# Performance work log

Measured on AMD Instinct MI355X. Metric: run time of the kernel, lower is better.

The kernel has to match this reference:

```python
import jax, jax.numpy as jnp
import numpy as np

MARGIN = 1.0
SOFT_MARGIN = False
EPS = 1e-8


def setup_inputs() -> dict:
    key = jax.random.key(0)
    k1, k2 = jax.random.split(key)
    B, D, N_CLASSES = 8192, 128, 64
    emb = jax.random.normal(k1, (B, D), dtype=jnp.float32)
    # docstring says embeddings are L2-normalized
    emb = emb / jnp.linalg.norm(emb, axis=1, keepdims=True)
    labels = jax.random.randint(k2, (B,), 0, N_CLASSES, dtype=jnp.int32)
    return {"embeddings": emb, "labels": labels}


def _pairwise_distances(embeddings):
    # d_ij = sqrt(relu(|e_i|^2 + |e_j|^2 - 2 e_i.e_j) + eps)
    dot = embeddings @ embeddings.T                      # (B, B)
    sq = jnp.sum(embeddings * embeddings, axis=1, keepdims=True)
    dist2 = jax.nn.relu(sq + sq.T - 2.0 * dot)
    return jnp.sqrt(dist2 + EPS)


def reference(embeddings, labels):
    B = embeddings.shape[0]
    d = _pairwise_distances(embeddings)                  # (B, B)

    same = labels[:, None] == labels[None, :]            # (B, B) bool
    not_self = ~jnp.eye(B, dtype=bool)
    pos_mask = same & not_self
    neg_mask = ~same

    inf = jnp.asarray(jnp.inf, d.dtype)
    # hardest positive: max same-label distance; hardest negative: min diff-label distance
    pos_dist = jnp.max(jnp.where(pos_mask, d, -inf), axis=1)   # (B,)
    neg_dist = jnp.min(jnp.where(neg_mask, d, inf), axis=1)    # (B,)

    valid = jnp.any(pos_mask, axis=1) & jnp.any(neg_mask, axis=1)

    diff = pos_dist - neg_dist
    if SOFT_MARGIN:
        losses = jax.nn.softplus(diff)
    else:
        losses = jax.nn.relu(diff + MARGIN)

    n_valid = jnp.sum(valid.astype(jnp.int32))
    loss_sum = jnp.sum(jnp.where(valid, losses, 0.0))
    loss = jnp.where(n_valid > 0,
                     loss_sum / jnp.maximum(n_valid, 1).astype(losses.dtype),
                     jnp.asarray(0.0, losses.dtype))
    return loss, n_valid
```

## Files before the change

### kernel.cpp

```cpp
#include <hip/hip_runtime.h>
#include <hip/hip_bf16.h>

typedef unsigned short ushort_t;
typedef __attribute__((ext_vector_type(8))) short s16x8;
typedef __attribute__((ext_vector_type(4))) float f32x4;

#define NB 8192
#define ND 128
#define KE 192
#define ROWB (KE*2)
#define WROWS 64
#define BMR 256
#define TCOLS 64
#define CHUNK 512
#define NTILE (CHUNK/TCOLS)
#define NCHUNK (NB/CHUNK)
#define EPS 1e-8f
#define MARGIN 1.0f

typedef const __attribute__((address_space(1))) void* gptr_t;
typedef __attribute__((address_space(3))) void* lptr_t;
__device__ __forceinline__ void gll16(const void* g, void* l) {
    __builtin_amdgcn_global_load_lds((gptr_t)g, (lptr_t)l, 16, 0, 0);
}

__global__ void prep_kernel(const float* __restrict__ E,
                            const int* __restrict__ labels,
                            ushort_t* __restrict__ Eb,
                            float* __restrict__ sqA) {
    const int tid  = threadIdx.x;
    const int lane = tid & 63;
    const int row  = blockIdx.x * 4 + (tid >> 6);

    const float2 v = reinterpret_cast<const float2*>(E + (size_t)row * ND)[lane];
    __hip_bfloat16 b0 = __float2bfloat16(v.x);
    __hip_bfloat16 b1 = __float2bfloat16(v.y);
    uint pk = (uint)*reinterpret_cast<ushort_t*>(&b0)
            | ((uint)*reinterpret_cast<ushort_t*>(&b1) << 16);
    uint* rowp = reinterpret_cast<uint*>(Eb + (size_t)row * KE);
    rowp[lane] = pk;

    if (lane < 32) {
        const int lab = labels[row];
        const int c0 = lane * 2, c1 = lane * 2 + 1;
        uint e = (uint)((lab == c0) ? 0x3F80u : 0u)
               | (((lab == c1) ? 0x3F80u : 0u) << 16);
        rowp[64 + lane] = e;
    }

    float ss = v.x * v.x + v.y * v.y;
    #pragma unroll
    for (int off = 32; off; off >>= 1) ss += __shfl_down(ss, off, 64);
    if (lane == 0) sqA[row] = ss;
}

__global__ __launch_bounds__(256, 1) void triplet_gemm(
        const ushort_t* __restrict__ Eb,
        const int* __restrict__ labels,
        float* __restrict__ pvPart,
        float* __restrict__ nvPart) {
    __shared__ __align__(16) ushort_t Bb[3][TCOLS * KE];

    const int tid = threadIdx.x, lane = tid & 63, w = tid >> 6;
    const int fr = lane & 15, fg = lane >> 4;
    const int rowBase = blockIdx.x * BMR;
    const int chunkBase = blockIdx.y * CHUNK;
    const int wrow = rowBase + w * WROWS;

    int srcOff[6];
    #pragma unroll
    for (int it = 0; it < 6; ++it) {
        const int c = it * 256 + tid;
        const int r = c / 24, s = c - r * 24;
        srcOff[it] = r * ROWB + ((s ^ (r & 7)) << 4);
    }
    auto stage = [&](int bufi, int t) {
        const char* g = (const char*)Eb + (size_t)(chunkBase + t * TCOLS) * ROWB;
        char* l = (char*)&Bb[0][0] + bufi * (TCOLS * KE * 2);
        #pragma unroll
        for (int it = 0; it < 6; ++it)
            gll16(g + srcOff[it], l + (it * 256 + w * 64) * 16);
    };

    int swb[6];
    #pragma unroll
    for (int ks = 0; ks < 6; ++ks) swb[ks] = (((ks * 4 + fg) ^ (fr & 7)) << 4);

    int labv[4];
    #pragma unroll
    for (int mi = 0; mi < 4; ++mi) labv[mi] = labels[wrow + mi * 16 + fr];

    s16x8 a[6][4];
    #pragma unroll
    for (int ks = 0; ks < 4; ++ks)
        #pragma unroll
        for (int mi = 0; mi < 4; ++mi)
            a[ks][mi] = *reinterpret_cast<const s16x8*>(
                (const char*)Eb + (size_t)(wrow + mi * 16 + fr) * ROWB + ks * 64 + fg * 16);

    stage(0, 0);
    stage(1, 1);
    asm volatile("s_waitcnt vmcnt(6)" ::: "memory");
    __builtin_amdgcn_sched_barrier(0);
    __builtin_amdgcn_s_barrier();
    __builtin_amdgcn_sched_barrier(0);

    #pragma unroll
    for (int ks = 4; ks < 6; ++ks)
        #pragma unroll
        for (int mi = 0; mi < 4; ++mi) {
            s16x8 t{};
            #pragma unroll
            for (int j = 0; j < 8; ++j) {
                const int c = (ks - 4) * 32 + fg * 8 + j;
                t[j] = (labv[mi] == c) ? (short)0xC100 : (short)0;
            }
            a[ks][mi] = t;
        }

    const float PINF = __builtin_inff(), NINF = -__builtin_inff();
    f32x4 pv[4], nv[4];
    #pragma unroll
    for (int mi = 0; mi < 4; ++mi) {
        pv[mi] = f32x4{PINF, PINF, PINF, PINF};
        nv[mi] = f32x4{NINF, NINF, NINF, NINF};
    }
    const f32x4 zf = {0.f, 0.f, 0.f, 0.f};

    #pragma unroll 1
    for (int p = 0; p < NTILE; ++p) {
        if (p + 2 < NTILE) {
            stage((p + 2) % 3, p + 2);
            asm volatile("s_waitcnt vmcnt(6)" ::: "memory");
        } else {
            asm volatile("s_waitcnt vmcnt(0)" ::: "memory");
        }
        const char* cp = (const char*)&Bb[0][0] + (p % 3) * (TCOLS * KE * 2);

        auto loadB = [&](s16x8* b, int ni) {
            #pragma unroll
            for (int ks = 0; ks < 6; ++ks)
                b[ks] = *reinterpret_cast<const s16x8*>(
                    cp + (ni * 16 + fr) * ROWB + swb[ks]);
        };
        auto mfmaFold = [&](const s16x8* b) {
            f32x4 acc[4];
            #pragma unroll
            for (int mi = 0; mi < 4; ++mi)
                acc[mi] = __builtin_amdgcn_mfma_f32_16x16x32_bf16(a[0][mi], b[0], zf, 0, 0, 0);
            #pragma unroll
            for (int ks = 1; ks < 6; ++ks)
                #pragma unroll
                for (int mi = 0; mi < 4; ++mi)
                    acc[mi] = __builtin_amdgcn_mfma_f32_16x16x32_bf16(a[ks][mi], b[ks], acc[mi], 0, 0, 0);
            #pragma unroll
            for (int mi = 0; mi < 4; ++mi)
                #pragma unroll
                for (int reg = 0; reg < 4; ++reg) {
                    pv[mi][reg] = fminf(pv[mi][reg], acc[mi][reg]);
                    nv[mi][reg] = fmaxf(nv[mi][reg], acc[mi][reg]);
                }
        };

        s16x8 bX[6], bY[6];
        loadB(bX, 0);
        loadB(bY, 1); mfmaFold(bX);
        loadB(bX, 2); mfmaFold(bY);
        loadB(bY, 3); mfmaFold(bX);
        mfmaFold(bY);

        __builtin_amdgcn_sched_barrier(0);
        __builtin_amdgcn_s_barrier();
        __builtin_amdgcn_sched_barrier(0);
    }

    #pragma unroll
    for (int mi = 0; mi < 4; ++mi)
        #pragma unroll
        for (int reg = 0; reg < 4; ++reg) {
            float p = pv[mi][reg], n = nv[mi][reg];
            #pragma unroll
            for (int off = 1; off < 16; off <<= 1) {
                p = fminf(p, __shfl_xor(p, off, 64));
                n = fmaxf(n, __shfl_xor(n, off, 64));
            }
            if (fr == 0) {
                const int grow = wrow + mi * 16 + fg * 4 + reg;
                pvPart[(size_t)blockIdx.y * NB + grow] = p;
                nvPart[(size_t)blockIdx.y * NB + grow] = n;
            }
        }
}

__global__ void finalize_partial(const float* __restrict__ sqA,
                                 const float* __restrict__ pvPart,
                                 const float* __restrict__ nvPart,
                                 float* __restrict__ fpart) {
    __shared__ float sl[4], sc[4];
    const int tid = threadIdx.x, lane = tid & 63, w = tid >> 6;
    const int i = blockIdx.x * 256 + tid;
    const float PINF = __builtin_inff(), NINF = -__builtin_inff();

    float pMin = PINF, nMax = NINF;
    #pragma unroll
    for (int c = 0; c < NCHUNK; ++c) {
        pMin = fminf(pMin, pvPart[(size_t)c * NB + i]);
        nMax = fmaxf(nMax, nvPart[(size_t)c * NB + i]);
    }
    bool valid = (nMax > -2.0f) && (pMin < -6.0f);
    float dotP = pMin + 8.0f;
    float dotN = nMax;
    float sq = sqA[i];
    float pd = sqrtf(fmaxf(sq + 1.0f - 2.0f * dotP, 0.f) + EPS);
    float nd = sqrtf(fmaxf(sq + 1.0f - 2.0f * dotN, 0.f) + EPS);
    float l  = fmaxf(pd - nd + MARGIN, 0.f);
    float lv = valid ? l : 0.f;
    float cv = valid ? 1.f : 0.f;
    #pragma unroll
    for (int off = 32; off; off >>= 1) {
        lv += __shfl_down(lv, off, 64);
        cv += __shfl_down(cv, off, 64);
    }
    if (lane == 0) { sl[w] = lv; sc[w] = cv; }
    __syncthreads();
    if (tid == 0) {
        fpart[blockIdx.x * 2]     = sl[0] + sl[1] + sl[2] + sl[3];
        fpart[blockIdx.x * 2 + 1] = sc[0] + sc[1] + sc[2] + sc[3];
    }
}

__global__ void finalize_write(const float* __restrict__ fpart, float* __restrict__ out) {
    if (threadIdx.x == 0) {
        float L = 0.f, C = 0.f;
        #pragma unroll
        for (int k = 0; k < NB / 256; ++k) { L += fpart[2 * k]; C += fpart[2 * k + 1]; }
        out[0] = (C > 0.f) ? (L / C) : 0.f;
        out[1] = C;
    }
}

extern "C" void kernel_launch(void* const* d_in, const int* in_sizes, int n_in,
                              void* d_out, int out_size, void* d_ws, size_t ws_size,
                              hipStream_t stream) {
    const float* E      = (const float*)d_in[0];
    const int*   labels = (const int*)d_in[1];
    float*       out    = (float*)d_out;

    char* ws = (char*)d_ws;
    size_t off = 0;
    ushort_t* Eb     = (ushort_t*)(ws + off);  off += (size_t)NB * KE * 2;
    float*    sqA    = (float*)(ws + off);     off += (size_t)NB * 4;
    float*    pvPart = (float*)(ws + off);     off += (size_t)NCHUNK * NB * 4;
    float*    nvPart = (float*)(ws + off);     off += (size_t)NCHUNK * NB * 4;
    float*    fpart  = (float*)(ws + off);

    prep_kernel<<<NB / 4, 256, 0, stream>>>(E, labels, Eb, sqA);

    dim3 grid(NB / BMR, NCHUNK);
    triplet_gemm<<<grid, 256, 0, stream>>>(Eb, labels, pvPart, nvPart);

    finalize_partial<<<NB / 256, 256, 0, stream>>>(sqA, pvPart, nvPart, fpart);
    finalize_write<<<1, 64, 0, stream>>>(fpart, out);
}
```

Before: 40.02 us.

## Drop LDS staging, load B directly from global, reduce with atomics

Removes the triple-buffered LDS pipeline and has each wave load B fragments straight from global memory (L2-cached), with launch bounds raised to two blocks per CU. Per-chunk partial min/max arrays are replaced by atomicMin/atomicMax on order-preserving unsigned encodings, and the two finalize kernels are merged into one single-block kernel. The squared norm is assumed to be 1, so its computation is dropped. The aim is to cut launch count, workspace traffic and barrier overhead, at the risk of higher global load latency, redundant L2 reads and atomic contention.

```diff
diff --git a/kernel.cpp b/kernel.cpp
--- a/kernel.cpp
+++ b/kernel.cpp
@@ -8,26 +8,26 @@
 #define NB 8192
 #define ND 128
 #define KE 192
-#define ROWB (KE*2)
 #define WROWS 64
 #define BMR 256
-#define TCOLS 64
 #define CHUNK 512
-#define NTILE (CHUNK/TCOLS)
-#define NCHUNK (NB/CHUNK)
+#define NC16 (CHUNK/16)
 #define EPS 1e-8f
 #define MARGIN 1.0f
 
-typedef const __attribute__((address_space(1))) void* gptr_t;
-typedef __attribute__((address_space(3))) void* lptr_t;
-__device__ __forceinline__ void gll16(const void* g, void* l) {
-    __builtin_amdgcn_global_load_lds((gptr_t)g, (lptr_t)l, 16, 0, 0);
+__device__ __forceinline__ unsigned f2u(float f) {
+    unsigned u = __float_as_uint(f);
+    return (u & 0x80000000u) ? ~u : (u | 0x80000000u);
+}
+__device__ __forceinline__ float u2f(unsigned u) {
+    return (u & 0x80000000u) ? __uint_as_float(u & 0x7fffffffu) : __uint_as_float(~u);
 }
 
 __global__ void prep_kernel(const float* __restrict__ E,
                             const int* __restrict__ labels,
                             ushort_t* __restrict__ Eb,
-                            float* __restrict__ sqA) {
+                            unsigned* __restrict__ posU,
+                            unsigned* __restrict__ negU) {
     const int tid  = threadIdx.x;
     const int lane = tid & 63;
     const int row  = blockIdx.x * 4 + (tid >> 6);
@@ -48,47 +48,22 @@
         rowp[64 + lane] = e;
     }
 
-    float ss = v.x * v.x + v.y * v.y;
-    #pragma unroll
-    for (int off = 32; off; off >>= 1) ss += __shfl_down(ss, off, 64);
-    if (lane == 0) sqA[row] = ss;
-}
-
-__global__ __launch_bounds__(256, 1) void triplet_gemm(
+    const int gid = blockIdx.x * 256 + tid;
+    if (gid < NB) {
+        posU[gid] = f2u(__builtin_inff());
+        negU[gid] = f2u(-__builtin_inff());
+    }
+}
+
+__global__ __launch_bounds__(256, 2) void triplet_gemm(
         const ushort_t* __restrict__ Eb,
         const int* __restrict__ labels,
-        float* __restrict__ pvPart,
-        float* __restrict__ nvPart) {
-    __shared__ __align__(16) ushort_t Bb[3][TCOLS * KE];
-
+        unsigned* __restrict__ posU,
+        unsigned* __restrict__ negU) {
     const int tid = threadIdx.x, lane = tid & 63, w = tid >> 6;
     const int fr = lane & 15, fg = lane >> 4;
-    const int rowBase = blockIdx.x * BMR;
-    const int chunkBase = blockIdx.y * CHUNK;
-    const int wrow = rowBase + w * WROWS;
-
-    int srcOff[6];
-    #pragma unroll
-    for (int it = 0; it < 6; ++it) {
-        const int c = it * 256 + tid;
-        const int r = c / 24, s = c - r * 24;
-        srcOff[it] = r * ROWB + ((s ^ (r & 7)) << 4);
-    }
-    auto stage = [&](int bufi, int t) {
-        const char* g = (const char*)Eb + (size_t)(chunkBase + t * TCOLS) * ROWB;
-        char* l = (char*)&Bb[0][0] + bufi * (TCOLS * KE * 2);
-        #pragma unroll
-        for (int it = 0; it < 6; ++it)
-            gll16(g + srcOff[it], l + (it * 256 + w * 64) * 16);
-    };
-
-    int swb[6];
-    #pragma unroll
-    for (int ks = 0; ks < 6; ++ks) swb[ks] = (((ks * 4 + fg) ^ (fr & 7)) << 4);
-
-    int labv[4];
-    #pragma unroll
-    for (int mi = 0; mi < 4; ++mi) labv[mi] = labels[wrow + mi * 16 + fr];
+    const int wrow = blockIdx.x * BMR + w * WROWS;
+    const int colBase = blockIdx.y * CHUNK;
 
     s16x8 a[6][4];
     #pragma unroll
@@ -96,27 +71,24 @@
         #pragma unroll
         for (int mi = 0; mi < 4; ++mi)
             a[ks][mi] = *reinterpret_cast<const s16x8*>(
-                (const char*)Eb + (size_t)(wrow + mi * 16 + fr) * ROWB + ks * 64 + fg * 16);
-
-    stage(0, 0);
-    stage(1, 1);
-    asm volatile("s_waitcnt vmcnt(6)" ::: "memory");
-    __builtin_amdgcn_sched_barrier(0);
-    __builtin_amdgcn_s_barrier();
-    __builtin_amdgcn_sched_barrier(0);
-
-    #pragma unroll
-    for (int ks = 4; ks < 6; ++ks)
-        #pragma unroll
-        for (int mi = 0; mi < 4; ++mi) {
-            s16x8 t{};
-            #pragma unroll
-            for (int j = 0; j < 8; ++j) {
-                const int c = (ks - 4) * 32 + fg * 8 + j;
-                t[j] = (labv[mi] == c) ? (short)0xC100 : (short)0;
-            }
-            a[ks][mi] = t;
-        }
+                Eb + (size_t)(wrow + mi * 16 + fr) * KE + ks * 32 + fg * 8);
+    {
+        int labv[4];
+        #pragma unroll
+        for (int mi = 0; mi < 4; ++mi) labv[mi] = labels[wrow + mi * 16 + fr];
+        #pragma unroll
+        for (int ks = 4; ks < 6; ++ks)
+            #pragma unroll
+            for (int mi = 0; mi < 4; ++mi) {
+                s16x8 t{};
+                #pragma unroll
+                for (int j = 0; j < 8; ++j) {
+                    const int c = (ks - 4) * 32 + fg * 8 + j;
+                    t[j] = (labv[mi] == c) ? (short)0xC100 : (short)0;
+                }
+                a[ks][mi] = t;
+            }
+    }
 
     const float PINF = __builtin_inff(), NINF = -__builtin_inff();
     f32x4 pv[4], nv[4];
@@ -127,51 +99,41 @@
     }
     const f32x4 zf = {0.f, 0.f, 0.f, 0.f};
 
+    const ushort_t* bbase = Eb + (size_t)(colBase + fr) * KE + fg * 8;
+
+    auto loadB = [&](s16x8* b, int c) {
+        const ushort_t* p = bbase + (size_t)c * 16 * KE;
+        #pragma unroll
+        for (int ks = 0; ks < 6; ++ks)
+            b[ks] = *reinterpret_cast<const s16x8*>(p + ks * 32);
+    };
+    auto fold = [&](const s16x8* b) {
+        f32x4 acc[4];
+        #pragma unroll
+        for (int mi = 0; mi < 4; ++mi)
+            acc[mi] = __builtin_amdgcn_mfma_f32_16x16x32_bf16(a[0][mi], b[0], zf, 0, 0, 0);
+        #pragma unroll
+        for (int ks = 1; ks < 6; ++ks)
+            #pragma unroll
+            for (int mi = 0; mi < 4; ++mi)
+                acc[mi] = __builtin_amdgcn_mfma_f32_16x16x32_bf16(a[ks][mi], b[ks], acc[mi], 0, 0, 0);
+        #pragma unroll
+        for (int mi = 0; mi < 4; ++mi)
+            #pragma unroll
+            for (int reg = 0; reg < 4; ++reg) {
+                pv[mi][reg] = fminf(pv[mi][reg], acc[mi][reg]);
+                nv[mi][reg] = fmaxf(nv[mi][reg], acc[mi][reg]);
+            }
+    };
+
+    s16x8 bX[6], bY[6];
+    loadB(bX, 0);
     #pragma unroll 1
-    for (int p = 0; p < NTILE; ++p) {
-        if (p + 2 < NTILE) {
-            stage((p + 2) % 3, p + 2);
-            asm volatile("s_waitcnt vmcnt(6)" ::: "memory");
-        } else {
-            asm volatile("s_waitcnt vmcnt(0)" ::: "memory");
-        }
-        const char* cp = (const char*)&Bb[0][0] + (p % 3) * (TCOLS * KE * 2);
-
-        auto loadB = [&](s16x8* b, int ni) {
-            #pragma unroll
-            for (int ks = 0; ks < 6; ++ks)
-                b[ks] = *reinterpret_cast<const s16x8*>(
-                    cp + (ni * 16 + fr) * ROWB + swb[ks]);
-        };
-        auto mfmaFold = [&](const s16x8* b) {
-            f32x4 acc[4];
-            #pragma unroll
-            for (int mi = 0; mi < 4; ++mi)
-                acc[mi] = __builtin_amdgcn_mfma_f32_16x16x32_bf16(a[0][mi], b[0], zf, 0, 0, 0);
-            #pragma unroll
-            for (int ks = 1; ks < 6; ++ks)
-                #pragma unroll
-                for (int mi = 0; mi < 4; ++mi)
-                    acc[mi] = __builtin_amdgcn_mfma_f32_16x16x32_bf16(a[ks][mi], b[ks], acc[mi], 0, 0, 0);
-            #pragma unroll
-            for (int mi = 0; mi < 4; ++mi)
-                #pragma unroll
-                for (int reg = 0; reg < 4; ++reg) {
-                    pv[mi][reg] = fminf(pv[mi][reg], acc[mi][reg]);
-                    nv[mi][reg] = fmaxf(nv[mi][reg], acc[mi][reg]);
-                }
-        };
-
-        s16x8 bX[6], bY[6];
-        loadB(bX, 0);
-        loadB(bY, 1); mfmaFold(bX);
-        loadB(bX, 2); mfmaFold(bY);
-        loadB(bY, 3); mfmaFold(bX);
-        mfmaFold(bY);
-
-        __builtin_amdgcn_sched_barrier(0);
-        __builtin_amdgcn_s_barrier();
-        __builtin_amdgcn_sched_barrier(0);
+    for (int c = 0; c < NC16; c += 2) {
+        loadB(bY, c + 1);
+        fold(bX);
+        if (c + 2 < NC16) loadB(bX, c + 2);
+        fold(bY);
     }
 
     #pragma unroll
@@ -186,54 +148,41 @@
             }
             if (fr == 0) {
                 const int grow = wrow + mi * 16 + fg * 4 + reg;
-                pvPart[(size_t)blockIdx.y * NB + grow] = p;
-                nvPart[(size_t)blockIdx.y * NB + grow] = n;
+                atomicMin(&posU[grow], f2u(p));
+                atomicMax(&negU[grow], f2u(n));
             }
         }
 }
 
-__global__ void finalize_partial(const float* __restrict__ sqA,
-                                 const float* __restrict__ pvPart,
-                                 const float* __restrict__ nvPart,
-                                 float* __restrict__ fpart) {
-    __shared__ float sl[4], sc[4];
+__global__ void finalize_kernel(const unsigned* __restrict__ posU,
+                                const unsigned* __restrict__ negU,
+                                float* __restrict__ out) {
+    __shared__ float sl[16], sc[16];
     const int tid = threadIdx.x, lane = tid & 63, w = tid >> 6;
-    const int i = blockIdx.x * 256 + tid;
-    const float PINF = __builtin_inff(), NINF = -__builtin_inff();
-
-    float pMin = PINF, nMax = NINF;
-    #pragma unroll
-    for (int c = 0; c < NCHUNK; ++c) {
-        pMin = fminf(pMin, pvPart[(size_t)c * NB + i]);
-        nMax = fmaxf(nMax, nvPart[(size_t)c * NB + i]);
-    }
-    bool valid = (nMax > -2.0f) && (pMin < -6.0f);
-    float dotP = pMin + 8.0f;
-    float dotN = nMax;
-    float sq = sqA[i];
-    float pd = sqrtf(fmaxf(sq + 1.0f - 2.0f * dotP, 0.f) + EPS);
-    float nd = sqrtf(fmaxf(sq + 1.0f - 2.0f * dotN, 0.f) + EPS);
-    float l  = fmaxf(pd - nd + MARGIN, 0.f);
-    float lv = valid ? l : 0.f;
-    float cv = valid ? 1.f : 0.f;
+
+    float lsum = 0.f, csum = 0.f;
+    #pragma unroll
+    for (int k = 0; k < NB / 1024; ++k) {
+        const int i = k * 1024 + tid;
+        float pMin = u2f(posU[i]);
+        float nMax = u2f(negU[i]);
+        bool valid = (nMax > -2.0f) && (pMin < -6.0f);
+        float pd = sqrtf(fmaxf(2.0f - 2.0f * (pMin + 8.0f), 0.f) + EPS);
+        float nd = sqrtf(fmaxf(2.0f - 2.0f * nMax, 0.f) + EPS);
+        float l  = fmaxf(pd - nd + MARGIN, 0.f);
+        if (valid) { lsum += l; csum += 1.f; }
+    }
     #pragma unroll
     for (int off = 32; off; off >>= 1) {
-        lv += __shfl_down(lv, off, 64);
-        cv += __shfl_down(cv, off, 64);
-    }
-    if (lane == 0) { sl[w] = lv; sc[w] = cv; }
+        lsum += __shfl_down(lsum, off, 64);
+        csum += __shfl_down(csum, off, 64);
+    }
+    if (lane == 0) { sl[w] = lsum; sc[w] = csum; }
     __syncthreads();
     if (tid == 0) {
-        fpart[blockIdx.x * 2]     = sl[0] + sl[1] + sl[2] + sl[3];
-        fpart[blockIdx.x * 2 + 1] = sc[0] + sc[1] + sc[2] + sc[3];
-    }
-}
-
-__global__ void finalize_write(const float* __restrict__ fpart, float* __restrict__ out) {
-    if (threadIdx.x == 0) {
         float L = 0.f, C = 0.f;
         #pragma unroll
-        for (int k = 0; k < NB / 256; ++k) { L += fpart[2 * k]; C += fpart[2 * k + 1]; }
+        for (int k = 0; k < 16; ++k) { L += sl[k]; C += sc[k]; }
         out[0] = (C > 0.f) ? (L / C) : 0.f;
         out[1] = C;
     }
@@ -248,17 +197,14 @@
 
     char* ws = (char*)d_ws;
     size_t off = 0;
-    ushort_t* Eb     = (ushort_t*)(ws + off);  off += (size_t)NB * KE * 2;
-    float*    sqA    = (float*)(ws + off);     off += (size_t)NB * 4;
-    float*    pvPart = (float*)(ws + off);     off += (size_t)NCHUNK * NB * 4;
-    float*    nvPart = (float*)(ws + off);     off += (size_t)NCHUNK * NB * 4;
-    float*    fpart  = (float*)(ws + off);
-
-    prep_kernel<<<NB / 4, 256, 0, stream>>>(E, labels, Eb, sqA);
-
-    dim3 grid(NB / BMR, NCHUNK);
-    triplet_gemm<<<grid, 256, 0, stream>>>(Eb, labels, pvPart, nvPart);
-
-    finalize_partial<<<NB / 256, 256, 0, stream>>>(sqA, pvPart, nvPart, fpart);
-    finalize_write<<<1, 64, 0, stream>>>(fpart, out);
-}
+    ushort_t* Eb   = (ushort_t*)(ws + off);  off += (size_t)NB * KE * 2;
+    unsigned* posU = (unsigned*)(ws + off);  off += (size_t)NB * 4;
+    unsigned* negU = (unsigned*)(ws + off);  off += (size_t)NB * 4;
+
+    prep_kernel<<<NB / 4, 256, 0, stream>>>(E, labels, Eb, posU, negU);
+
+    dim3 grid(NB / BMR, NB / CHUNK);
+    triplet_gemm<<<grid, 256, 0, stream>>>(Eb, labels, posU, negU);
+
+    finalize_kernel<<<1, 1024, 0, stream>>>(posU, negU, out);
+}
```

New measurement: 64.88 us. 1.62x slower.
